# Optimization experiments

Hardware: AMD Instinct MI355X
Metric: run time of the kernel (lower is better)

Reference implementation:

```python
import jax, jax.numpy as jnp
import numpy as np

NUM_CLASSES = 128
NUM_DOMAINS = 6
FEAT_DIM = 256
B = 524288
MOMENTUM = 0.9
MARGIN = 1.0


def setup_inputs() -> dict:
    key = jax.random.key(0)
    k1, k2, k3, k4, k5, k6 = jax.random.split(key, 6)
    mu_tilde = jax.random.normal(k1, (B, FEAT_DIM), dtype=jnp.float32)
    anchors = jax.random.normal(k2, (NUM_DOMAINS, NUM_CLASSES, FEAT_DIM), dtype=jnp.float32)
    domain_means = jax.random.normal(k3, (NUM_DOMAINS, FEAT_DIM), dtype=jnp.float32)
    domain_vars = jax.random.uniform(k4, (NUM_DOMAINS, FEAT_DIM), dtype=jnp.float32)
    y_true = jax.random.randint(k5, (B,), 0, NUM_CLASSES, dtype=jnp.int32)
    d_true = jax.random.randint(k6, (B,), 0, NUM_DOMAINS, dtype=jnp.int32)
    return {"mu_tilde": mu_tilde, "anchors": anchors, "domain_means": domain_means,
            "domain_vars": domain_vars, "y_true": y_true, "d_true": d_true}


def reference(mu_tilde, anchors, domain_means, domain_vars, y_true, d_true):
    m = MOMENTUM
    one = jnp.asarray(1.0, mu_tilde.dtype)

    # ---- update(): fused per-(domain,class) segment mean + EMA anchor write ----
    seg = d_true.astype(jnp.int32) * NUM_CLASSES + y_true.astype(jnp.int32)
    n_seg = NUM_DOMAINS * NUM_CLASSES
    seg_sum = jax.ops.segment_sum(mu_tilde, seg, num_segments=n_seg)          # (Nd*C, D)
    seg_cnt = jax.ops.segment_sum(jnp.ones((B,), mu_tilde.dtype), seg, num_segments=n_seg)
    seg_mean = seg_sum / jnp.maximum(seg_cnt, one)[:, None]
    has_samples = (seg_cnt > 0).reshape(NUM_DOMAINS, NUM_CLASSES, 1)
    batch_anchor = seg_mean.reshape(NUM_DOMAINS, NUM_CLASSES, FEAT_DIM)
    new_anchors = jnp.where(has_samples, m * anchors + (1.0 - m) * batch_anchor, anchors)

    # ---- update(): per-domain mean/var (unbiased) + EMA ----
    d_sum = jax.ops.segment_sum(mu_tilde, d_true, num_segments=NUM_DOMAINS)
    d_sq = jax.ops.segment_sum(mu_tilde * mu_tilde, d_true, num_segments=NUM_DOMAINS)
    d_cnt = jax.ops.segment_sum(jnp.ones((B,), mu_tilde.dtype), d_true, num_segments=NUM_DOMAINS)
    safe_cnt = jnp.maximum(d_cnt, one)[:, None]
    b_mean = d_sum / safe_cnt
    b_var = (d_sq - safe_cnt * b_mean * b_mean) / jnp.maximum(d_cnt - 1.0, one)[:, None]
    g = (d_cnt > 1)[:, None]
    new_means = jnp.where(g, m * domain_means + (1.0 - m) * b_mean, domain_means)
    new_vars = jnp.where(g, m * domain_vars + (1.0 - m) * b_var, domain_vars)

    # ---- caa_loss() on updated anchors (all anchors initialized) ----
    class_mean = new_anchors.mean(axis=0, keepdims=True)                      # (1, C, D)
    loss_intra = jnp.mean((new_anchors - class_mean) ** 2)                    # avg of per-class MSE
    A_mean = new_anchors.mean(axis=0)                                         # (C, D)
    sq = jnp.sum(A_mean * A_mean, axis=1)
    d2 = sq[:, None] + sq[None, :] - 2.0 * (A_mean @ A_mean.T)
    off_diag = ~jnp.eye(NUM_CLASSES, dtype=bool)
    d2_safe = jnp.where(off_diag, jnp.maximum(d2, 1e-12), 1.0)
    dist = jnp.sqrt(d2_safe)
    loss_inter = jnp.sum(jnp.where(off_diag, jax.nn.relu(MARGIN - dist), 0.0))
    loss_inter = loss_inter / (NUM_CLASSES * (NUM_CLASSES - 1))
    loss_caa = loss_intra + loss_inter

    # ---- stats_align_loss() on updated stats ----
    global_mean = new_means.mean(axis=0)
    global_var = new_vars.mean(axis=0)
    loss_mean = jnp.mean((new_means - global_mean) ** 2)   # sum_d mse / Nd
    loss_var = jnp.mean((new_vars - global_var) ** 2)
    mu_mean = mu_tilde.mean(axis=0)
    mu_var = jnp.mean(mu_tilde * mu_tilde, axis=0) - mu_mean * mu_mean        # biased var
    loss_mu_mean = jnp.mean((mu_mean - global_mean) ** 2)
    loss_mu_var = jnp.mean((mu_var - global_var) ** 2)
    loss_stats = loss_mean + loss_var + loss_mu_mean + loss_mu_var

    return new_anchors, new_means, new_vars, loss_caa + loss_stats
```

## Files before the change

kernel.cpp:

```cpp
#include <hip/hip_runtime.h>

#define B_N   524288
#define FEAT  256
#define NC    128
#define ND    6
#define NSEG  768
#define CAP   1024

#define ZERO_WORDS 36620

typedef float f4v __attribute__((ext_vector_type(4)));

__device__ __forceinline__ float block_reduce(float v, float* lds) {
  #pragma unroll
  for (int o = 32; o > 0; o >>= 1) v += __shfl_down(v, o, 64);
  int wid = threadIdx.x >> 6, lane = threadIdx.x & 63;
  if (lane == 0) lds[wid] = v;
  __syncthreads();
  int nw = (blockDim.x + 63) >> 6;
  v = 0.0f;
  if (wid == 0 && lane < nw) v = lds[lane];
  if (wid == 0) {
    #pragma unroll
    for (int o = 4; o > 0; o >>= 1) v += __shfl_down(v, o, 64);
  }
  return v;
}

#define SCHUNK 4096
#define SCAT_BLOCKS (B_N / SCHUNK)
__global__ __launch_bounds__(1024)
void scatter_k(const int* __restrict__ y, const int* __restrict__ dmn,
               int* __restrict__ cursor, int* __restrict__ slots) {
  __shared__ int lcnt[NSEG];
  __shared__ int lbase[NSEG];
  int t = threadIdx.x;
  if (t < NSEG) lcnt[t] = 0;
  __syncthreads();
  int base = blockIdx.x * SCHUNK;
  int segr[4], lposr[4];
  #pragma unroll
  for (int k = 0; k < 4; ++k) {
    int i = base + t + k * 1024;
    int seg = dmn[i] * NC + y[i];
    segr[k] = seg;
    lposr[k] = atomicAdd(&lcnt[seg], 1);
  }
  __syncthreads();
  if (t < NSEG) lbase[t] = atomicAdd(&cursor[t], lcnt[t]);
  __syncthreads();
  #pragma unroll
  for (int k = 0; k < 4; ++k) {
    int i = base + t + k * 1024;
    int p = lbase[segr[k]] + lposr[k];
    if (p < CAP) slots[segr[k] * CAP + p] = i;
  }
}

__global__ __launch_bounds__(512, 6)
void segreduce_k(const float* __restrict__ mu, const int* __restrict__ slots,
                 const int* __restrict__ cursor, const float* __restrict__ anchors,
                 float* __restrict__ out_anchors, float* __restrict__ class_mean,
                 float* __restrict__ d_sum_acc, float* __restrict__ d_sq_acc,
                 float* __restrict__ d_cnt) {
  int seg = blockIdx.x;
  int cnt = cursor[seg];
  if (cnt > CAP) cnt = CAP;
  int dom = seg >> 7;
  int cls = seg & 127;
  int t  = threadIdx.x;
  int rr = t >> 6;
  int dq = t & 63;
  const int* sl = slots + seg * CAP;
  const size_t doff = (size_t)(dq << 2);

  int c0 = (cnt * rr) >> 3;
  int c1 = (cnt * (rr + 1)) >> 3;

  float ax=0,ay=0,az=0,aw=0, aqx=0,aqy=0,aqz=0,aqw=0;
  float bx=0,by=0,bz=0,bw=0, bqx=0,bqy=0,bqz=0,bqw=0;

  int r = c0;
  int row0 = (r     < c1) ? sl[r]     : 0;
  int row1 = (r + 1 < c1) ? sl[r + 1] : 0;
  while (r + 1 < c1) {
    int n0 = (r + 2 < c1) ? sl[r + 2] : 0;
    int n1 = (r + 3 < c1) ? sl[r + 3] : 0;
    const f4v v0 = __builtin_nontemporal_load(
        reinterpret_cast<const f4v*>(mu + (size_t)row0 * FEAT + doff));
    const f4v v1 = __builtin_nontemporal_load(
        reinterpret_cast<const f4v*>(mu + (size_t)row1 * FEAT + doff));
    ax += v0.x; ay += v0.y; az += v0.z; aw += v0.w;
    aqx += v0.x*v0.x; aqy += v0.y*v0.y; aqz += v0.z*v0.z; aqw += v0.w*v0.w;
    bx += v1.x; by += v1.y; bz += v1.z; bw += v1.w;
    bqx += v1.x*v1.x; bqy += v1.y*v1.y; bqz += v1.z*v1.z; bqw += v1.w*v1.w;
    r += 2; row0 = n0; row1 = n1;
  }
  if (r < c1) {
    const f4v v0 = __builtin_nontemporal_load(
        reinterpret_cast<const f4v*>(mu + (size_t)row0 * FEAT + doff));
    ax += v0.x; ay += v0.y; az += v0.z; aw += v0.w;
    aqx += v0.x*v0.x; aqy += v0.y*v0.y; aqz += v0.z*v0.z; aqw += v0.w*v0.w;
  }
  ax += bx; ay += by; az += bz; aw += bw;
  aqx += bqx; aqy += bqy; aqz += bqz; aqw += bqw;

  __shared__ float4 redS[512];
  __shared__ float4 redQ[512];
  redS[t] = make_float4(ax, ay, az, aw);
  redQ[t] = make_float4(aqx, aqy, aqz, aqw);
  float4 aold;
  if (rr == 0) aold = *reinterpret_cast<const float4*>(anchors + (size_t)seg * FEAT + doff);
  __syncthreads();
  if (rr == 0) {
    float4 s = redS[t], q = redQ[t];
    #pragma unroll
    for (int g = 1; g < 8; ++g) {
      float4 a = redS[t + 64*g]; s.x+=a.x; s.y+=a.y; s.z+=a.z; s.w+=a.w;
      float4 b = redQ[t + 64*g]; q.x+=b.x; q.y+=b.y; q.z+=b.z; q.w+=b.w;
    }
    float inv01 = 0.1f / fmaxf((float)cnt, 1.0f);
    float4 o;
    if (cnt > 0) {
      o.x = 0.9f*aold.x + s.x*inv01; o.y = 0.9f*aold.y + s.y*inv01;
      o.z = 0.9f*aold.z + s.z*inv01; o.w = 0.9f*aold.w + s.w*inv01;
    } else o = aold;
    *reinterpret_cast<float4*>(out_anchors + (size_t)seg * FEAT + doff) = o;

    int cbase = cls * FEAT + (dq << 2);
    const float s6 = 1.0f / 6.0f;
    atomicAdd(&class_mean[cbase+0], o.x*s6); atomicAdd(&class_mean[cbase+1], o.y*s6);
    atomicAdd(&class_mean[cbase+2], o.z*s6); atomicAdd(&class_mean[cbase+3], o.w*s6);

    int base = dom * FEAT + (dq << 2);
    atomicAdd(&d_sum_acc[base+0], s.x); atomicAdd(&d_sum_acc[base+1], s.y);
    atomicAdd(&d_sum_acc[base+2], s.z); atomicAdd(&d_sum_acc[base+3], s.w);
    atomicAdd(&d_sq_acc[base+0], q.x);  atomicAdd(&d_sq_acc[base+1], q.y);
    atomicAdd(&d_sq_acc[base+2], q.z);  atomicAdd(&d_sq_acc[base+3], q.w);
  }
  if (t == 0) atomicAdd(&d_cnt[dom], (float)cnt);
}

__global__ __launch_bounds__(256)
void tail_k(const float* __restrict__ class_mean, const float* __restrict__ out_anchors,
            const float* __restrict__ dmeans, const float* __restrict__ dvars,
            const float* __restrict__ d_sum_acc, const float* __restrict__ d_sq_acc,
            const float* __restrict__ d_cnt, float* __restrict__ out_means,
            float* __restrict__ out_vars, float* __restrict__ loss_acc,
            int* __restrict__ done_ctr, float* __restrict__ out_loss) {
  int b = blockIdx.x;
  int t = threadIdx.x;
  __shared__ float rbuf[8];

  if (b < NC) {
    __shared__ float Ai[FEAT];
    __shared__ float dots[256];
    __shared__ float sq2[256];
    float cmb = class_mean[b * FEAT + t];
    Ai[t] = cmb;
    float li = 0.0f;
    #pragma unroll
    for (int dom = 0; dom < ND; ++dom) {
      float a = out_anchors[(size_t)(dom * NC + b) * FEAT + t];
      float e = a - cmb; li += e * e;
    }
    __syncthreads();
    int j = t & 127, h = t >> 7;
    const float* Aj  = class_mean + (size_t)j * FEAT + h * 128;
    const float* Aih = Ai + h * 128;
    float dot = 0.0f, sj = 0.0f;
    #pragma unroll 8
    for (int k = 0; k < 128; ++k) { float a = Aj[k]; dot += Aih[k] * a; sj += a * a; }
    dots[t] = dot; sq2[t] = sj;
    __syncthreads();
    float contrib = 0.0f;
    if (h == 0 && j != b) {
      float sqb = sq2[b] + sq2[b + 128];
      float sqj = sq2[j] + sq2[j + 128];
      float d2 = sqb + sqj - 2.0f * (dots[j] + dots[j + 128]);
      d2 = fmaxf(d2, 1e-12f);
      contrib = fmaxf(1.0f - sqrtf(d2), 0.0f);
    }
    float r1 = block_reduce(li, rbuf);
    __syncthreads();
    float r2 = block_reduce(contrib, rbuf);
    if (t == 0) { atomicAdd(&loss_acc[0], r1); atomicAdd(&loss_acc[1], r2); }
  } else {
    int d = t;
    float nm[ND], nv[ND];
    float gm = 0.0f, gv = 0.0f, tsum = 0.0f, tsq = 0.0f;
    #pragma unroll
    for (int dom = 0; dom < ND; ++dom) {
      float cf = d_cnt[dom];
      float safe = fmaxf(cf, 1.0f);
      float su = d_sum_acc[dom * FEAT + d];
      float sq = d_sq_acc[dom * FEAT + d];
      tsum += su; tsq += sq;
      float bm = su / safe;
      float bv = (sq - safe * bm * bm) / fmaxf(cf - 1.0f, 1.0f);
      float m0 = dmeans[dom * FEAT + d], v0 = dvars[dom * FEAT + d];
      bool g = cf > 1.0f;
      float m1 = g ? (0.9f * m0 + 0.1f * bm) : m0;
      float v1 = g ? (0.9f * v0 + 0.1f * bv) : v0;
      out_means[dom * FEAT + d] = m1;
      out_vars[dom * FEAT + d]  = v1;
      nm[dom] = m1; nv[dom] = v1; gm += m1; gv += v1;
    }
    gm /= 6.0f; gv /= 6.0f;
    float lm = 0.0f, lv = 0.0f;
    #pragma unroll
    for (int dom = 0; dom < ND; ++dom) {
      float e = nm[dom] - gm; lm += e * e;
      float f = nv[dom] - gv; lv += f * f;
    }
    float mum = tsum * (1.0f / (float)B_N);
    float muv = tsq * (1.0f / (float)B_N) - mum * mum;
    float lmm = (mum - gm) * (mum - gm);
    float lmv = (muv - gv) * (muv - gv);
    float val = (lm + lv) * (1.0f / 1536.0f) + (lmm + lmv) * (1.0f / 256.0f);
    float r = block_reduce(val, rbuf);
    if (t == 0) atomicAdd(&loss_acc[2], r);
  }

  if (t == 0) {
    __threadfence();
    int old = atomicAdd(done_ctr, 1);
    if (old == NC) {
      float li = atomicAdd(&loss_acc[0], 0.0f);
      float le = atomicAdd(&loss_acc[1], 0.0f);
      float ls = atomicAdd(&loss_acc[2], 0.0f);
      *out_loss = li * (1.0f / 196608.0f)
                + le * (1.0f / 16256.0f)
                + ls;
    }
  }
}

extern "C" void kernel_launch(void* const* d_in, const int* in_sizes, int n_in,
                              void* d_out, int out_size, void* d_ws, size_t ws_size,
                              hipStream_t stream) {
  const float* mu      = (const float*)d_in[0];
  const float* anchors = (const float*)d_in[1];
  const float* dmeans  = (const float*)d_in[2];
  const float* dvars   = (const float*)d_in[3];
  const int*   y       = (const int*)d_in[4];
  const int*   dmn     = (const int*)d_in[5];

  float* out = (float*)d_out;
  float* out_anchors = out;
  float* out_means   = out + 196608;
  float* out_vars    = out + 198144;
  float* out_loss    = out + 199680;

  float* wsf       = (float*)d_ws;
  int*   cursor    = (int*)d_ws;
  float* d_cnt     = wsf + 768;
  float* d_sum_acc = wsf + 776;
  float* d_sq_acc  = wsf + 2312;
  float* loss_acc  = wsf + 3848;
  int*   done_ctr  = (int*)d_ws + 3851;
  float* class_mean= wsf + 3852;
  int*   slots     = (int*)(wsf + ZERO_WORDS);

  hipMemsetAsync(d_ws, 0, ZERO_WORDS * sizeof(float), stream);
  scatter_k  <<<SCAT_BLOCKS, 1024, 0, stream>>>(y, dmn, cursor, slots);
  segreduce_k<<<NSEG, 512, 0, stream>>>(mu, slots, cursor, anchors, out_anchors, class_mean,
                                        d_sum_acc, d_sq_acc, d_cnt);
  tail_k     <<<NC + 1, 256, 0, stream>>>(class_mean, out_anchors, dmeans, dvars,
                                          d_sum_acc, d_sq_acc, d_cnt,
                                          out_means, out_vars, loss_acc, done_ctr, out_loss);
}
```

Baseline: 130.9 us.

## Vectorize scatter index loads, fold workspace zeroing into scatter, drop nontemporal loads

The scatter kernel now reads four labels per thread with int4 loads and runs as 128 blocks. It also takes over zeroing of the accumulator workspace, so the memset only clears the 768 cursors. The segment-reduce kernel switches from nontemporal loads to plain float4 loads of mu. This removes memset traffic and some index-load overhead, but lets mu rows go through the cache normally, which may change L2 behaviour on the gather.

New measurement: 133.9 us. 2.3% more time.

```diff
diff --git a/kernel.cpp b/kernel.cpp
--- a/kernel.cpp
+++ b/kernel.cpp
@@ -7,7 +7,7 @@
 #define NSEG  768
 #define CAP   1024
 
-#define ZERO_WORDS 36620
+#define ZWORDS_SCATTER 35852
 
 typedef float f4v __attribute__((ext_vector_type(4)));
 
@@ -27,34 +27,35 @@
   return v;
 }
 
-#define SCHUNK 4096
-#define SCAT_BLOCKS (B_N / SCHUNK)
+#define SCAT_BLOCKS 128
 __global__ __launch_bounds__(1024)
 void scatter_k(const int* __restrict__ y, const int* __restrict__ dmn,
-               int* __restrict__ cursor, int* __restrict__ slots) {
+               int* __restrict__ cursor, int* __restrict__ slots,
+               float* __restrict__ zbase ) {
   __shared__ int lcnt[NSEG];
   __shared__ int lbase[NSEG];
   int t = threadIdx.x;
+  int gid = blockIdx.x * 1024 + t;
+  if (gid < ZWORDS_SCATTER) zbase[gid] = 0.0f;
   if (t < NSEG) lcnt[t] = 0;
   __syncthreads();
-  int base = blockIdx.x * SCHUNK;
-  int segr[4], lposr[4];
-  #pragma unroll
-  for (int k = 0; k < 4; ++k) {
-    int i = base + t + k * 1024;
-    int seg = dmn[i] * NC + y[i];
-    segr[k] = seg;
-    lposr[k] = atomicAdd(&lcnt[seg], 1);
-  }
+
+  const int4 yy = reinterpret_cast<const int4*>(y)[gid];
+  const int4 dd = reinterpret_cast<const int4*>(dmn)[gid];
+  int seg0 = dd.x * NC + yy.x, seg1 = dd.y * NC + yy.y;
+  int seg2 = dd.z * NC + yy.z, seg3 = dd.w * NC + yy.w;
+  int p0 = atomicAdd(&lcnt[seg0], 1);
+  int p1 = atomicAdd(&lcnt[seg1], 1);
+  int p2 = atomicAdd(&lcnt[seg2], 1);
+  int p3 = atomicAdd(&lcnt[seg3], 1);
   __syncthreads();
   if (t < NSEG) lbase[t] = atomicAdd(&cursor[t], lcnt[t]);
   __syncthreads();
-  #pragma unroll
-  for (int k = 0; k < 4; ++k) {
-    int i = base + t + k * 1024;
-    int p = lbase[segr[k]] + lposr[k];
-    if (p < CAP) slots[segr[k] * CAP + p] = i;
-  }
+  int i0 = gid * 4;
+  p0 += lbase[seg0]; if (p0 < CAP) slots[seg0 * CAP + p0] = i0;
+  p1 += lbase[seg1]; if (p1 < CAP) slots[seg1 * CAP + p1] = i0 + 1;
+  p2 += lbase[seg2]; if (p2 < CAP) slots[seg2 * CAP + p2] = i0 + 2;
+  p3 += lbase[seg3]; if (p3 < CAP) slots[seg3 * CAP + p3] = i0 + 3;
 }
 
 __global__ __launch_bounds__(512, 6)
@@ -86,10 +87,8 @@
   while (r + 1 < c1) {
     int n0 = (r + 2 < c1) ? sl[r + 2] : 0;
     int n1 = (r + 3 < c1) ? sl[r + 3] : 0;
-    const f4v v0 = __builtin_nontemporal_load(
-        reinterpret_cast<const f4v*>(mu + (size_t)row0 * FEAT + doff));
-    const f4v v1 = __builtin_nontemporal_load(
-        reinterpret_cast<const f4v*>(mu + (size_t)row1 * FEAT + doff));
+    const float4 v0 = *reinterpret_cast<const float4*>(mu + (size_t)row0 * FEAT + doff);
+    const float4 v1 = *reinterpret_cast<const float4*>(mu + (size_t)row1 * FEAT + doff);
     ax += v0.x; ay += v0.y; az += v0.z; aw += v0.w;
     aqx += v0.x*v0.x; aqy += v0.y*v0.y; aqz += v0.z*v0.z; aqw += v0.w*v0.w;
     bx += v1.x; by += v1.y; bz += v1.z; bw += v1.w;
@@ -97,8 +96,7 @@
     r += 2; row0 = n0; row1 = n1;
   }
   if (r < c1) {
-    const f4v v0 = __builtin_nontemporal_load(
-        reinterpret_cast<const f4v*>(mu + (size_t)row0 * FEAT + doff));
+    const float4 v0 = *reinterpret_cast<const float4*>(mu + (size_t)row0 * FEAT + doff);
     ax += v0.x; ay += v0.y; az += v0.z; aw += v0.w;
     aqx += v0.x*v0.x; aqy += v0.y*v0.y; aqz += v0.z*v0.z; aqw += v0.w*v0.w;
   }
@@ -260,10 +258,10 @@
   float* loss_acc  = wsf + 3848;
   int*   done_ctr  = (int*)d_ws + 3851;
   float* class_mean= wsf + 3852;
-  int*   slots     = (int*)(wsf + ZERO_WORDS);
-
-  hipMemsetAsync(d_ws, 0, ZERO_WORDS * sizeof(float), stream);
-  scatter_k  <<<SCAT_BLOCKS, 1024, 0, stream>>>(y, dmn, cursor, slots);
+  int*   slots     = (int*)(wsf + 36620);
+
+  hipMemsetAsync(cursor, 0, NSEG * sizeof(int), stream);
+  scatter_k  <<<SCAT_BLOCKS, 1024, 0, stream>>>(y, dmn, cursor, slots, wsf + 768);
   segreduce_k<<<NSEG, 512, 0, stream>>>(mu, slots, cursor, anchors, out_anchors, class_mean,
                                         d_sum_acc, d_sq_acc, d_cnt);
   tail_k     <<<NC + 1, 256, 0, stream>>>(class_mean, out_anchors, dmeans, dvars,
```
